# Kernel tuning notes

Measured on AMD Instinct MI355X. Metric: run time of the kernel, lower is better.

The kernel has to match this reference:

```python
import jax, jax.numpy as jnp
import numpy as np

N = 100_000      # nodes
E = 1_600_000    # edges (avg degree 16)
C_IN, C_H, C_OUT = 32, 64, 64
G = 64           # graphs in batch


def setup_inputs() -> dict:
    key = jax.random.key(0)
    ks = jax.random.split(key, 10)
    x = jax.random.normal(ks[0], (N, C_IN), jnp.float32)
    edge_index = jax.random.randint(ks[1], (2, E), 0, N, dtype=jnp.int64)
    edge_weight = jax.random.uniform(ks[2], (E,), jnp.float32)
    batch = jnp.sort(jax.random.randint(ks[3], (N,), 0, G, dtype=jnp.int64))
    def lin(k, fan_in, fan_out):
        return jax.random.normal(k, (fan_in, fan_out), jnp.float32) / np.float32(np.sqrt(fan_in))
    W1 = lin(ks[4], C_IN, C_H)
    W2 = lin(ks[5], C_H, C_H)
    W3 = lin(ks[6], C_H, C_OUT)
    b1 = jnp.zeros((C_H,), jnp.float32)
    b2 = jnp.zeros((C_H,), jnp.float32)
    b3 = jnp.zeros((C_OUT,), jnp.float32)
    return {"x": x, "edge_weight": edge_weight, "W1": W1, "b1": b1,
            "W2": W2, "b2": b2, "W3": W3, "b3": b3,
            "edge_index": edge_index, "batch": batch}


def _gcn_norm(edge_index, edge_weight, n):
    # PyG GCNConv default: add self-loops (weight 1), symmetric D^-1/2 A D^-1/2 norm.
    loop = jnp.arange(n, dtype=edge_index.dtype)
    src = jnp.concatenate([edge_index[0], loop])
    dst = jnp.concatenate([edge_index[1], loop])
    ew = jnp.concatenate([edge_weight, jnp.ones((n,), edge_weight.dtype)])
    deg = jax.ops.segment_sum(ew, dst, num_segments=n)
    dis = jnp.where(deg > 0, jax.lax.rsqrt(deg), jnp.float32(0))
    norm = dis[src] * ew * dis[dst]
    return src, dst, norm


def _gcn_layer(h, W, b, src, dst, norm, n):
    h = h @ W                                 # [N, out]
    msg = h[src] * norm[:, None]              # gather + scale  [E+N, out]
    agg = jax.ops.segment_sum(msg, dst, num_segments=n)
    return agg + b


def reference(x, edge_weight, W1, b1, W2, b2, W3, b3, edge_index, batch):
    n = x.shape[0]
    src, dst, norm = _gcn_norm(edge_index, edge_weight, n)  # shared across layers
    h = jax.nn.silu(_gcn_layer(x, W1, b1, src, dst, norm, n))
    # Dropout(0.1) is identity in eval mode
    h = jax.nn.silu(_gcn_layer(h, W2, b2, src, dst, norm, n))
    h = jax.nn.silu(_gcn_layer(h, W3, b3, src, dst, norm, n))
    # global_mean_pool over graphs
    sums = jax.ops.segment_sum(h, batch, num_segments=G)
    counts = jax.ops.segment_sum(jnp.ones((n,), h.dtype), batch, num_segments=G)
    return sums / jnp.maximum(counts, 1)[:, None]
```

## Files before the change

### kernel.cpp

```cpp
#include <hip/hip_runtime.h>
#include <hip/hip_fp16.h>
#include <math.h>


#define NB   256
#define PBLK 1024
#define FIXP_SCALE 1048576.0f
#define FIXP_MASK  ((1ULL << 40) - 1)

__device__ __forceinline__ int lower_bound_i(const int* __restrict__ a, int n, int v) {
    int lo = 0, hi = n;
    while (lo < hi) {
        int m = (lo + hi) >> 1;
        if (a[m] < v) lo = m + 1; else hi = m;
    }
    return lo;
}

__global__ __launch_bounds__(256) void k_bhist(const int* __restrict__ dst,
                                               int* __restrict__ hcnt, int e) {
    __shared__ int hist[NB];
    int tid = threadIdx.x, blk = blockIdx.x;
    hist[tid] = 0;
    __syncthreads();
    int chunk = (e + PBLK - 1) / PBLK;
    int lo = blk * chunk, hi = min(e, lo + chunk);
    for (int i = lo + tid; i < hi; i += 256)
        atomicAdd(&hist[dst[i] >> 9], 1);
    __syncthreads();
    hcnt[tid * PBLK + blk] = hist[tid];
}

__global__ __launch_bounds__(256) void k_bscan(int* __restrict__ hcnt,
                                               int* __restrict__ btot) {
    __shared__ int s[256];
    int b = blockIdx.x, tid = threadIdx.x;
    int* row = hcnt + b * PBLK;
    int a0 = row[4 * tid], a1 = row[4 * tid + 1], a2 = row[4 * tid + 2], a3 = row[4 * tid + 3];
    int tsum = a0 + a1 + a2 + a3;
    s[tid] = tsum;
    __syncthreads();
    for (int off = 1; off < 256; off <<= 1) {
        int t = (tid >= off) ? s[tid - off] : 0;
        __syncthreads();
        s[tid] += t;
        __syncthreads();
    }
    int ex = s[tid] - tsum;
    row[4 * tid] = ex;
    row[4 * tid + 1] = ex + a0;
    row[4 * tid + 2] = ex + a0 + a1;
    row[4 * tid + 3] = ex + a0 + a1 + a2;
    if (tid == 255) btot[b] = s[255];
}

__global__ __launch_bounds__(256) void k_bbase(const int* __restrict__ btot,
                                               int* __restrict__ bbase,
                                               int* __restrict__ rowptr, int n, int e) {
    __shared__ int s[256];
    int tid = threadIdx.x;
    int v = btot[tid];
    s[tid] = v;
    __syncthreads();
    for (int off = 1; off < 256; off <<= 1) {
        int t = (tid >= off) ? s[tid - off] : 0;
        __syncthreads();
        s[tid] += t;
        __syncthreads();
    }
    bbase[tid] = s[tid] - v;
    if (tid == 255) bbase[NB] = s[255];
    if (tid == 0) rowptr[n] = e;
}

__global__ __launch_bounds__(256) void k_bpart(const int* __restrict__ src,
                                               const int* __restrict__ dst,
                                               const float* __restrict__ ew,
                                               const int* __restrict__ hcnt,
                                               const int* __restrict__ bbase,
                                               int2* __restrict__ bedge, int e) {
    __shared__ int cur[NB];
    int tid = threadIdx.x, blk = blockIdx.x;
    cur[tid] = bbase[tid] + hcnt[tid * PBLK + blk];
    __syncthreads();
    int chunk = (e + PBLK - 1) / PBLK;
    int lo = blk * chunk, hi = min(e, lo + chunk);
    for (int i = lo + tid; i < hi; i += 256) {
        int d = dst[i];
        int pos = atomicAdd(&cur[d >> 9], 1);
        bedge[pos] = make_int2(src[i] | ((d & 511) << 17), __float_as_int(ew[i]));
    }
}

__global__ __launch_bounds__(256) void k_bucket(const int2* __restrict__ bedge,
                                                const int* __restrict__ bbase,
                                                float* __restrict__ dis,
                                                int* __restrict__ rowptr,
                                                int2* __restrict__ em, int n) {
    __shared__ unsigned long long pk[512];
    __shared__ int cnt[512];
    __shared__ int scn[512];
    __shared__ float sdis[512];
    __shared__ int cur[512];
    int b = blockIdx.x, tid = threadIdx.x;
    int e0 = bbase[b], e1 = bbase[b + 1];
    pk[tid] = 0ULL; pk[tid + 256] = 0ULL;
    __syncthreads();
    for (int i = e0 + tid; i < e1; i += 256) {
        int2 v = bedge[i];
        int dlo = (v.x >> 17) & 511;
        unsigned long long p =
            (1ULL << 40) | (unsigned long long)(__int_as_float(v.y) * FIXP_SCALE);
        atomicAdd(&pk[dlo], p);
    }
    __syncthreads();
#pragma unroll
    for (int k = 0; k < 2; ++k) {
        int i = tid + k * 256;
        unsigned long long v = pk[i];
        int c = (int)(v >> 40);
        cnt[i] = c; scn[i] = c;
        sdis[i] = rsqrtf(1.0f + (float)(v & FIXP_MASK) * (1.0f / FIXP_SCALE));
    }
    __syncthreads();
    for (int off = 1; off < 512; off <<= 1) {
        int i0 = tid, i1 = tid + 256;
        int v0 = (i0 >= off) ? scn[i0 - off] : 0;
        int v1 = (i1 >= off) ? scn[i1 - off] : 0;
        __syncthreads();
        scn[i0] += v0; scn[i1] += v1;
        __syncthreads();
    }
#pragma unroll
    for (int k = 0; k < 2; ++k) {
        int i = tid + k * 256;
        int rb = e0 + scn[i] - cnt[i];
        cur[i] = rb;
        int node = (b << 9) + i;
        if (node < n) { rowptr[node] = rb; dis[node] = sdis[i]; }
    }
    __syncthreads();
    for (int i = e0 + tid; i < e1; i += 256) {
        int2 v = bedge[i];
        int dlo = (v.x >> 17) & 511;
        int pos = atomicAdd(&cur[dlo], 1);
        float w = __int_as_float(v.y) * sdis[dlo];
        em[pos] = make_int2(v.x & 0x1FFFF, __float_as_int(w));
    }
}

__global__ void k_scale(const float* __restrict__ x, const float* __restrict__ dis,
                        __half* __restrict__ hs, int total) {
    int idx = blockIdx.x * blockDim.x + threadIdx.x;
    if (idx < total) hs[idx] = __float2half(x[idx] * dis[idx >> 5]);
}

__device__ __forceinline__ float2 cvt_pair(unsigned int u) {
    __half2 h2 = *(__half2*)&u;
    return __half22float2(h2);
}

__global__ __launch_bounds__(256, 2) void k_mm64(const __half* __restrict__ y,
                                                 const float* __restrict__ W,
                                                 __half* __restrict__ z, int n) {
    __shared__ float sw[64 * 64];
#pragma unroll
    for (int i = 0; i < 16; ++i)
        sw[threadIdx.x + 256 * i] = W[threadIdx.x + 256 * i];
    __syncthreads();
    int node = blockIdx.x * 256 + threadIdx.x;
    if (node >= n) return;
    uint4 yp[8];
    const uint4* yrow = (const uint4*)(y + (size_t)node * 64);
#pragma unroll
    for (int i = 0; i < 8; ++i) yp[i] = yrow[i];
    const unsigned int* ypk = (const unsigned int*)yp;
    float o[64];
#pragma unroll
    for (int j = 0; j < 64; ++j) o[j] = 0.0f;
#pragma unroll
    for (int k2 = 0; k2 < 32; ++k2) {
        float2 yk = cvt_pair(ypk[k2]);
        const float4* r0 = (const float4*)&sw[(2 * k2) * 64];
        const float4* r1 = (const float4*)&sw[(2 * k2 + 1) * 64];
#pragma unroll
        for (int j4 = 0; j4 < 16; ++j4) {
            float4 w0 = r0[j4];
            float4 w1 = r1[j4];
            o[4 * j4 + 0] = fmaf(yk.y, w1.x, fmaf(yk.x, w0.x, o[4 * j4 + 0]));
            o[4 * j4 + 1] = fmaf(yk.y, w1.y, fmaf(yk.x, w0.y, o[4 * j4 + 1]));
            o[4 * j4 + 2] = fmaf(yk.y, w1.z, fmaf(yk.x, w0.z, o[4 * j4 + 2]));
            o[4 * j4 + 3] = fmaf(yk.y, w1.w, fmaf(yk.x, w0.w, o[4 * j4 + 3]));
        }
    }
    __half2* zrow = (__half2*)(z + (size_t)node * 64);
#pragma unroll
    for (int j2 = 0; j2 < 32; ++j2)
        zrow[j2] = __float22half2_rn(make_float2(o[2 * j2], o[2 * j2 + 1]));
}

template <bool SCALE, typename OUT>
__global__ __launch_bounds__(256, 4) void k_agg64(const __half* __restrict__ z,
                                                  const int2* __restrict__ em,
                                                  const int* __restrict__ rowptr,
                                                  const float* __restrict__ dis,
                                                  const float* __restrict__ bias,
                                                  OUT* __restrict__ out, int n) {
    __shared__ __align__(8) int2 sme[4][64];
    int lane = threadIdx.x & 63, wv = threadIdx.x >> 6;
    int c = lane & 31, half = lane >> 5;
    const unsigned int* h32 = (const unsigned int*)z;
    float2 bv2 = ((const float2*)bias)[c];
    int wid = (blockIdx.x * blockDim.x + threadIdx.x) >> 6;
    int nw = (gridDim.x * blockDim.x) >> 6;
    for (int node = wid; node < n; node += nw) {
        int lo = rowptr[node], hi = rowptr[node + 1];
        int deg = hi - lo;
        float di = 0.0f;
        float2 acc = make_float2(0.0f, 0.0f);
        if (half == 0) {
            di = dis[node];
            float2 hv = cvt_pair(h32[(unsigned)(node * 32 + c)]);
            acc.x = di * hv.x; acc.y = di * hv.y;
        }
        for (int jb = 0; jb < deg; jb += 64) {
            int idx = lo + jb + lane;
            int2 me = (idx < hi) ? em[idx] : make_int2(0, 0);
            sme[wv][lane] = me;
            int rem = deg - jb;
#pragma unroll
            for (int g = 0; g < 4; ++g) {
                if (g * 16 < rem) {
                    int2 ev[8];
#pragma unroll
                    for (int t = 0; t < 8; ++t)
                        ev[t] = sme[wv][g * 16 + 2 * t + half];
                    unsigned int hv[8];
#pragma unroll
                    for (int t = 0; t < 8; ++t)
                        hv[t] = h32[(unsigned)(ev[t].x * 32 + c)];
#pragma unroll
                    for (int t = 0; t < 8; ++t) {
                        float ww = __int_as_float(ev[t].y);
                        float2 hf = cvt_pair(hv[t]);
                        acc.x = fmaf(ww, hf.x, acc.x);
                        acc.y = fmaf(ww, hf.y, acc.y);
                    }
                }
            }
        }
        acc.x += __shfl_down(acc.x, 32, 64);
        acc.y += __shfl_down(acc.y, 32, 64);
        if (half == 0) {
            float ox = acc.x + bv2.x, oy = acc.y + bv2.y;
            ox = ox / (1.0f + __expf(-ox));
            oy = oy / (1.0f + __expf(-oy));
            if (SCALE) { ox *= di; oy *= di; }
            if (sizeof(OUT) == 2) {
                ((__half2*)out)[(size_t)node * 32 + c] =
                    __float22half2_rn(make_float2(ox, oy));
            } else {
                ((float2*)out)[(size_t)node * 32 + c] = make_float2(ox, oy);
            }
        }
    }
}

__global__ __launch_bounds__(256, 3) void k_aggmm32(const __half* __restrict__ h,
                                                    const int2* __restrict__ em,
                                                    const int* __restrict__ rowptr,
                                                    const float* __restrict__ dis,
                                                    const float* __restrict__ W,
                                                    const float* __restrict__ bias,
                                                    __half* __restrict__ out, int n) {
    __shared__ __align__(16) float sacc[4][32];
    __shared__ __align__(8) int2 sme[4][64];
    int lane = threadIdx.x & 63, wv = threadIdx.x >> 6;
    int c = lane & 15, quarter = lane >> 4;
    const unsigned int* h32 = (const unsigned int*)h;
    float w[32];
#pragma unroll
    for (int k = 0; k < 32; ++k) w[k] = W[k * 64 + lane];
    float bv = bias[lane];
    int wid = (blockIdx.x * blockDim.x + threadIdx.x) >> 6;
    int nw = (gridDim.x * blockDim.x) >> 6;
    for (int node = wid; node < n; node += nw) {
#pragma unroll
        for (int k = 0; k < 32; ++k) asm volatile("" : "+v"(w[k]));
        int lo = rowptr[node], hi = rowptr[node + 1];
        int deg = hi - lo;
        float2 acc = make_float2(0.0f, 0.0f);
        if (quarter == 0) {
            float2 hv0 = cvt_pair(h32[(unsigned)(node * 16 + c)]);
            float di = dis[node];
            acc.x = di * hv0.x; acc.y = di * hv0.y;
        }
        for (int jb = 0; jb < deg; jb += 64) {
            int idx = lo + jb + lane;
            int2 me = (idx < hi) ? em[idx] : make_int2(0, 0);
            sme[wv][lane] = me;
            int rem = deg - jb;
#pragma unroll
            for (int g = 0; g < 4; ++g) {
                if (g * 16 < rem) {
                    int2 ev[4];
#pragma unroll
                    for (int t = 0; t < 4; ++t)
                        ev[t] = sme[wv][g * 16 + 4 * t + quarter];
                    unsigned int hv[4];
#pragma unroll
                    for (int t = 0; t < 4; ++t)
                        hv[t] = h32[(unsigned)(ev[t].x * 16 + c)];
#pragma unroll
                    for (int t = 0; t < 4; ++t) {
                        float ww = __int_as_float(ev[t].y);
                        float2 hf = cvt_pair(hv[t]);
                        acc.x = fmaf(ww, hf.x, acc.x);
                        acc.y = fmaf(ww, hf.y, acc.y);
                    }
                }
            }
        }
        acc.x += __shfl_down(acc.x, 32, 64);
        acc.y += __shfl_down(acc.y, 32, 64);
        acc.x += __shfl_down(acc.x, 16, 64);
        acc.y += __shfl_down(acc.y, 16, 64);
        if (quarter == 0) ((float2*)sacc[wv])[c] = acc;
        float o = bv;
        const float4* s4 = (const float4*)sacc[wv];
#pragma unroll
        for (int k4 = 0; k4 < 8; ++k4) {
            float4 a4 = s4[k4];
            o = fmaf(a4.x, w[4 * k4 + 0], o);
            o = fmaf(a4.y, w[4 * k4 + 1], o);
            o = fmaf(a4.z, w[4 * k4 + 2], o);
            o = fmaf(a4.w, w[4 * k4 + 3], o);
        }
        o = o / (1.0f + __expf(-o));
        o *= dis[node];
        out[(size_t)node * 64 + lane] = __float2half(o);
    }
}

__global__ void k_pool_partial(const float* __restrict__ h, const int* __restrict__ batch,
                               float* __restrict__ acc, int n) {
    int c = threadIdx.x & 63, r = threadIdx.x >> 6;
    int base = blockIdx.x * 128;
    int end = base + 128; if (end > n) end = n;
    float part = 0.0f;
    int cur = -1;
    for (int i = base + r; i < end; i += 4) {
        int g = batch[i];
        if (g != cur) {
            if (cur >= 0) atomicAdd(&acc[cur * 64 + c], part);
            part = 0.0f;
            cur = g;
        }
        part += h[(size_t)i * 64 + c];
    }
    if (cur >= 0) atomicAdd(&acc[cur * 64 + c], part);
}

__global__ void k_pool_final(const float* __restrict__ acc, const int* __restrict__ batch,
                             float* __restrict__ out, int n) {
    int idx = blockIdx.x * blockDim.x + threadIdx.x;
    int g = idx >> 6;
    int lo = lower_bound_i(batch, n, g);
    int hi = lower_bound_i(batch, n, g + 1);
    int cnt = hi - lo;
    out[idx] = acc[idx] / (float)(cnt > 0 ? cnt : 1);
}

extern "C" void kernel_launch(void* const* d_in, const int* in_sizes, int n_in,
                              void* d_out, int out_size, void* d_ws, size_t ws_size,
                              hipStream_t stream) {
    const float* x   = (const float*)d_in[0];
    const float* ew  = (const float*)d_in[1];
    const float* W1  = (const float*)d_in[2];
    const float* b1  = (const float*)d_in[3];
    const float* W2  = (const float*)d_in[4];
    const float* b2  = (const float*)d_in[5];
    const float* W3  = (const float*)d_in[6];
    const float* b3  = (const float*)d_in[7];
    const int*   eidx  = (const int*)d_in[8];
    const int*   batch = (const int*)d_in[9];
    float* out = (float*)d_out;

    const int E = in_sizes[1];
    const int N = in_sizes[9];
    const int G = 64;
    const int* src = eidx;
    const int* dst = eidx + E;

    char* p = (char*)d_ws;
    __half* A     = (__half*)p;                p += (size_t)N * 64 * sizeof(__half);
    __half* B     = (__half*)p;                p += (size_t)N * 64 * sizeof(__half);
    float* C      = (float*)p;                 p += (size_t)N * 64 * sizeof(float);
    float* dis    = (float*)p;                 p += (size_t)N * sizeof(float);
    int*   rowptr = (int*)p;                   p += (size_t)(N + 1) * sizeof(int);
    int*   bbase  = (int*)p;                   p += (size_t)(NB + 1) * sizeof(int);
    float* acc    = (float*)p;                 p += (size_t)G * 64 * sizeof(float);
    p = (char*)(((uintptr_t)p + 7) & ~(uintptr_t)7);
    int2*  em     = (int2*)p;

    int2* bedge = (int2*)A;
    int*  hcnt  = (int*)B;
    int*  btot  = (int*)B + NB * PBLK;

    const int BT = 256;
    const int FUSED_BLOCKS = 3125;
    const int MM_BLOCKS = (N + 255) / 256;

    k_bhist<<<PBLK, 256, 0, stream>>>(dst, hcnt, E);
    k_bscan<<<NB, 256, 0, stream>>>(hcnt, btot);
    k_bbase<<<1, 256, 0, stream>>>(btot, bbase, rowptr, N, E);
    k_bpart<<<PBLK, 256, 0, stream>>>(src, dst, ew, hcnt, bbase, bedge, E);
    k_bucket<<<NB, 256, 0, stream>>>(bedge, bbase, dis, rowptr, em, N);

    k_scale<<<(N * 32 + BT - 1) / BT, BT, 0, stream>>>(x, dis, (__half*)B, N * 32);
    k_aggmm32<<<FUSED_BLOCKS, BT, 0, stream>>>((__half*)B, em, rowptr, dis, W1, b1, A, N);

    k_mm64<<<MM_BLOCKS, BT, 0, stream>>>(A, W2, B, N);
    k_agg64<true, __half><<<FUSED_BLOCKS, BT, 0, stream>>>(B, em, rowptr, dis, b2, A, N);

    k_mm64<<<MM_BLOCKS, BT, 0, stream>>>(A, W3, B, N);
    k_agg64<false, float><<<FUSED_BLOCKS, BT, 0, stream>>>(B, em, rowptr, dis, b3, C, N);

    hipMemsetAsync(acc, 0, (size_t)G * 64 * sizeof(float), stream);
    k_pool_partial<<<(N + 127) / 128, BT, 0, stream>>>(C, batch, acc, N);
    k_pool_final<<<(G * 64) / BT, BT, 0, stream>>>(acc, batch, out, N);
}
```

Measured before the change: 355.8 us.

## Batch 8 consecutive nodes per wave with shared edge window; split layer-1 agg and matmul

Aggregation kernels now give each wave a contiguous run of 8 nodes. Row pointers are loaded once per wave, and a 128-entry edge window in shared memory is reused across node boundaries, so short adjacency lists no longer waste a whole 64-edge load per node. The fused layer-1 aggregate+matmul kernel is replaced by a separate 32-channel aggregation that writes fp16 to a scratch buffer, followed by a per-node matmul with bias, SiLU and degree scaling. The split adds an extra kernel launch and an intermediate round trip through memory, in exchange for removing the per-node register-resident weight dot product from the gather loop.

New measurement: 364.6 us. 1.02x slower.

```diff
diff --git a/kernel.cpp b/kernel.cpp
--- a/kernel.cpp
+++ b/kernel.cpp
@@ -160,26 +160,100 @@
     return __half22float2(h2);
 }
 
-__global__ __launch_bounds__(256, 2) void k_mm64(const __half* __restrict__ y,
-                                                 const float* __restrict__ W,
-                                                 __half* __restrict__ z, int n) {
-    __shared__ float sw[64 * 64];
-#pragma unroll
-    for (int i = 0; i < 16; ++i)
+__global__ __launch_bounds__(256, 4) void k_agg32(const __half* __restrict__ hs,
+                                                  const int2* __restrict__ em,
+                                                  const int* __restrict__ rowptr,
+                                                  const float* __restrict__ dis,
+                                                  __half* __restrict__ y0, int n) {
+    __shared__ __align__(8) int2 sme[4][128];
+    int lane = threadIdx.x & 63, wv = threadIdx.x >> 6;
+    int c = lane & 15, quarter = lane >> 4;
+    const unsigned int* h32 = (const unsigned int*)hs;
+    int wid = (blockIdx.x * blockDim.x + threadIdx.x) >> 6;
+    int n0 = wid * 8;
+    if (n0 >= n) return;
+    int cnt = min(8, n - n0);
+    int rp = 0;
+    if (lane <= cnt) rp = rowptr[n0 + lane];
+    int hiw = __shfl(rp, cnt, 64);
+    int wlo = 0, whi = 0;
+    for (int k = 0; k < cnt; ++k) {
+        int node = n0 + k;
+        int lo = __shfl(rp, k, 64), hi = __shfl(rp, k + 1, 64);
+        float2 acc = make_float2(0.0f, 0.0f);
+        if (quarter == 0) {
+            float di = dis[node];
+            float2 hv = cvt_pair(h32[(unsigned)(node * 16 + c)]);
+            acc.x = di * hv.x; acc.y = di * hv.y;
+        }
+        int idx = lo;
+        while (idx < hi) {
+            if (idx >= whi) {
+                int i0 = idx + lane;
+                if (i0 < hiw) sme[wv][lane] = em[i0];
+                if (idx + 64 < hiw) {
+                    int i1 = i0 + 64;
+                    if (i1 < hiw) sme[wv][lane + 64] = em[i1];
+                }
+                wlo = idx; whi = idx + 128;
+            }
+            int base = idx - wlo;
+            int take = min(hi, whi) - idx;
+            for (int g = 0; g < take; g += 16) {
+                int2 ev[4]; unsigned int hv[4]; int pr[4];
+#pragma unroll
+                for (int t = 0; t < 4; ++t) {
+                    int p = g + 4 * t + quarter;
+                    pr[t] = p < take;
+                    int pc = pr[t] ? p : 0;
+                    ev[t] = sme[wv][base + pc];
+                }
+#pragma unroll
+                for (int t = 0; t < 4; ++t)
+                    hv[t] = h32[(unsigned)(ev[t].x * 16 + c)];
+#pragma unroll
+                for (int t = 0; t < 4; ++t) {
+                    float ww = pr[t] ? __int_as_float(ev[t].y) : 0.0f;
+                    float2 hf = cvt_pair(hv[t]);
+                    acc.x = fmaf(ww, hf.x, acc.x);
+                    acc.y = fmaf(ww, hf.y, acc.y);
+                }
+            }
+            idx += take;
+        }
+        acc.x += __shfl_down(acc.x, 32, 64);
+        acc.y += __shfl_down(acc.y, 32, 64);
+        acc.x += __shfl_down(acc.x, 16, 64);
+        acc.y += __shfl_down(acc.y, 16, 64);
+        if (quarter == 0)
+            ((__half2*)y0)[(size_t)node * 16 + c] =
+                __float22half2_rn(make_float2(acc.x, acc.y));
+    }
+}
+
+__global__ __launch_bounds__(256, 2) void k_mm32act(const __half* __restrict__ y0,
+                                                    const float* __restrict__ W,
+                                                    const float* __restrict__ bias,
+                                                    const float* __restrict__ dis,
+                                                    __half* __restrict__ out, int n) {
+    __shared__ __align__(16) float sw[32 * 64 + 64];
+#pragma unroll
+    for (int i = 0; i < 8; ++i)
         sw[threadIdx.x + 256 * i] = W[threadIdx.x + 256 * i];
+    if (threadIdx.x < 64) sw[2048 + threadIdx.x] = bias[threadIdx.x];
     __syncthreads();
     int node = blockIdx.x * 256 + threadIdx.x;
     if (node >= n) return;
-    uint4 yp[8];
-    const uint4* yrow = (const uint4*)(y + (size_t)node * 64);
-#pragma unroll
-    for (int i = 0; i < 8; ++i) yp[i] = yrow[i];
+    uint4 yp[4];
+    const uint4* yrow = (const uint4*)(y0 + (size_t)node * 32);
+#pragma unroll
+    for (int i = 0; i < 4; ++i) yp[i] = yrow[i];
     const unsigned int* ypk = (const unsigned int*)yp;
     float o[64];
 #pragma unroll
-    for (int j = 0; j < 64; ++j) o[j] = 0.0f;
-#pragma unroll
-    for (int k2 = 0; k2 < 32; ++k2) {
+    for (int j = 0; j < 64; ++j) o[j] = sw[2048 + j];
+#pragma unroll
+    for (int k2 = 0; k2 < 16; ++k2) {
         float2 yk = cvt_pair(ypk[k2]);
         const float4* r0 = (const float4*)&sw[(2 * k2) * 64];
         const float4* r1 = (const float4*)&sw[(2 * k2 + 1) * 64];
@@ -193,6 +267,50 @@
             o[4 * j4 + 3] = fmaf(yk.y, w1.w, fmaf(yk.x, w0.w, o[4 * j4 + 3]));
         }
     }
+    float dsc = dis[node];
+    __half2* orow = (__half2*)(out + (size_t)node * 64);
+#pragma unroll
+    for (int j2 = 0; j2 < 32; ++j2) {
+        float ox = o[2 * j2], oy = o[2 * j2 + 1];
+        ox = ox / (1.0f + __expf(-ox)) * dsc;
+        oy = oy / (1.0f + __expf(-oy)) * dsc;
+        orow[j2] = __float22half2_rn(make_float2(ox, oy));
+    }
+}
+
+__global__ __launch_bounds__(256, 2) void k_mm64(const __half* __restrict__ y,
+                                                 const float* __restrict__ W,
+                                                 __half* __restrict__ z, int n) {
+    __shared__ __align__(16) float sw[64 * 64];
+#pragma unroll
+    for (int i = 0; i < 16; ++i)
+        sw[threadIdx.x + 256 * i] = W[threadIdx.x + 256 * i];
+    __syncthreads();
+    int node = blockIdx.x * 256 + threadIdx.x;
+    if (node >= n) return;
+    uint4 yp[8];
+    const uint4* yrow = (const uint4*)(y + (size_t)node * 64);
+#pragma unroll
+    for (int i = 0; i < 8; ++i) yp[i] = yrow[i];
+    const unsigned int* ypk = (const unsigned int*)yp;
+    float o[64];
+#pragma unroll
+    for (int j = 0; j < 64; ++j) o[j] = 0.0f;
+#pragma unroll
+    for (int k2 = 0; k2 < 32; ++k2) {
+        float2 yk = cvt_pair(ypk[k2]);
+        const float4* r0 = (const float4*)&sw[(2 * k2) * 64];
+        const float4* r1 = (const float4*)&sw[(2 * k2 + 1) * 64];
+#pragma unroll
+        for (int j4 = 0; j4 < 16; ++j4) {
+            float4 w0 = r0[j4];
+            float4 w1 = r1[j4];
+            o[4 * j4 + 0] = fmaf(yk.y, w1.x, fmaf(yk.x, w0.x, o[4 * j4 + 0]));
+            o[4 * j4 + 1] = fmaf(yk.y, w1.y, fmaf(yk.x, w0.y, o[4 * j4 + 1]));
+            o[4 * j4 + 2] = fmaf(yk.y, w1.z, fmaf(yk.x, w0.z, o[4 * j4 + 2]));
+            o[4 * j4 + 3] = fmaf(yk.y, w1.w, fmaf(yk.x, w0.w, o[4 * j4 + 3]));
+        }
+    }
     __half2* zrow = (__half2*)(z + (size_t)node * 64);
 #pragma unroll
     for (int j2 = 0; j2 < 32; ++j2)
@@ -206,16 +324,22 @@
                                                   const float* __restrict__ dis,
                                                   const float* __restrict__ bias,
                                                   OUT* __restrict__ out, int n) {
-    __shared__ __align__(8) int2 sme[4][64];
+    __shared__ __align__(8) int2 sme[4][128];
     int lane = threadIdx.x & 63, wv = threadIdx.x >> 6;
     int c = lane & 31, half = lane >> 5;
     const unsigned int* h32 = (const unsigned int*)z;
     float2 bv2 = ((const float2*)bias)[c];
     int wid = (blockIdx.x * blockDim.x + threadIdx.x) >> 6;
-    int nw = (gridDim.x * blockDim.x) >> 6;
-    for (int node = wid; node < n; node += nw) {
-        int lo = rowptr[node], hi = rowptr[node + 1];
-        int deg = hi - lo;
+    int n0 = wid * 8;
+    if (n0 >= n) return;
+    int cnt = min(8, n - n0);
+    int rp = 0;
+    if (lane <= cnt) rp = rowptr[n0 + lane];
+    int hiw = __shfl(rp, cnt, 64);
+    int wlo = 0, whi = 0;
+    for (int k = 0; k < cnt; ++k) {
+        int node = n0 + k;
+        int lo = __shfl(rp, k, 64), hi = __shfl(rp, k + 1, 64);
         float di = 0.0f;
         float2 acc = make_float2(0.0f, 0.0f);
         if (half == 0) {
@@ -223,31 +347,40 @@
             float2 hv = cvt_pair(h32[(unsigned)(node * 32 + c)]);
             acc.x = di * hv.x; acc.y = di * hv.y;
         }
-        for (int jb = 0; jb < deg; jb += 64) {
-            int idx = lo + jb + lane;
-            int2 me = (idx < hi) ? em[idx] : make_int2(0, 0);
-            sme[wv][lane] = me;
-            int rem = deg - jb;
-#pragma unroll
-            for (int g = 0; g < 4; ++g) {
-                if (g * 16 < rem) {
-                    int2 ev[8];
-#pragma unroll
-                    for (int t = 0; t < 8; ++t)
-                        ev[t] = sme[wv][g * 16 + 2 * t + half];
-                    unsigned int hv[8];
-#pragma unroll
-                    for (int t = 0; t < 8; ++t)
-                        hv[t] = h32[(unsigned)(ev[t].x * 32 + c)];
-#pragma unroll
-                    for (int t = 0; t < 8; ++t) {
-                        float ww = __int_as_float(ev[t].y);
-                        float2 hf = cvt_pair(hv[t]);
-                        acc.x = fmaf(ww, hf.x, acc.x);
-                        acc.y = fmaf(ww, hf.y, acc.y);
-                    }
-                }
+        int idx = lo;
+        while (idx < hi) {
+            if (idx >= whi) {
+                int i0 = idx + lane;
+                if (i0 < hiw) sme[wv][lane] = em[i0];
+                if (idx + 64 < hiw) {
+                    int i1 = i0 + 64;
+                    if (i1 < hiw) sme[wv][lane + 64] = em[i1];
+                }
+                wlo = idx; whi = idx + 128;
             }
+            int base = idx - wlo;
+            int take = min(hi, whi) - idx;
+            for (int g = 0; g < take; g += 16) {
+                int2 ev[8]; unsigned int hv[8]; int pr[8];
+#pragma unroll
+                for (int t = 0; t < 8; ++t) {
+                    int p = g + 2 * t + half;
+                    pr[t] = p < take;
+                    int pc = pr[t] ? p : 0;
+                    ev[t] = sme[wv][base + pc];
+                }
+#pragma unroll
+                for (int t = 0; t < 8; ++t)
+                    hv[t] = h32[(unsigned)(ev[t].x * 32 + c)];
+#pragma unroll
+                for (int t = 0; t < 8; ++t) {
+                    float ww = pr[t] ? __int_as_float(ev[t].y) : 0.0f;
+                    float2 hf = cvt_pair(hv[t]);
+                    acc.x = fmaf(ww, hf.x, acc.x);
+                    acc.y = fmaf(ww, hf.y, acc.y);
+                }
+            }
+            idx += take;
         }
         acc.x += __shfl_down(acc.x, 32, 64);
         acc.y += __shfl_down(acc.y, 32, 64);
@@ -263,82 +396,6 @@
                 ((float2*)out)[(size_t)node * 32 + c] = make_float2(ox, oy);
             }
         }
-    }
-}
-
-__global__ __launch_bounds__(256, 3) void k_aggmm32(const __half* __restrict__ h,
-                                                    const int2* __restrict__ em,
-                                                    const int* __restrict__ rowptr,
-                                                    const float* __restrict__ dis,
-                                                    const float* __restrict__ W,
-                                                    const float* __restrict__ bias,
-                                                    __half* __restrict__ out, int n) {
-    __shared__ __align__(16) float sacc[4][32];
-    __shared__ __align__(8) int2 sme[4][64];
-    int lane = threadIdx.x & 63, wv = threadIdx.x >> 6;
-    int c = lane & 15, quarter = lane >> 4;
-    const unsigned int* h32 = (const unsigned int*)h;
-    float w[32];
-#pragma unroll
-    for (int k = 0; k < 32; ++k) w[k] = W[k * 64 + lane];
-    float bv = bias[lane];
-    int wid = (blockIdx.x * blockDim.x + threadIdx.x) >> 6;
-    int nw = (gridDim.x * blockDim.x) >> 6;
-    for (int node = wid; node < n; node += nw) {
-#pragma unroll
-        for (int k = 0; k < 32; ++k) asm volatile("" : "+v"(w[k]));
-        int lo = rowptr[node], hi = rowptr[node + 1];
-        int deg = hi - lo;
-        float2 acc = make_float2(0.0f, 0.0f);
-        if (quarter == 0) {
-            float2 hv0 = cvt_pair(h32[(unsigned)(node * 16 + c)]);
-            float di = dis[node];
-            acc.x = di * hv0.x; acc.y = di * hv0.y;
-        }
-        for (int jb = 0; jb < deg; jb += 64) {
-            int idx = lo + jb + lane;
-            int2 me = (idx < hi) ? em[idx] : make_int2(0, 0);
-            sme[wv][lane] = me;
-            int rem = deg - jb;
-#pragma unroll
-            for (int g = 0; g < 4; ++g) {
-                if (g * 16 < rem) {
-                    int2 ev[4];
-#pragma unroll
-                    for (int t = 0; t < 4; ++t)
-                        ev[t] = sme[wv][g * 16 + 4 * t + quarter];
-                    unsigned int hv[4];
-#pragma unroll
-                    for (int t = 0; t < 4; ++t)
-                        hv[t] = h32[(unsigned)(ev[t].x * 16 + c)];
-#pragma unroll
-                    for (int t = 0; t < 4; ++t) {
-                        float ww = __int_as_float(ev[t].y);
-                        float2 hf = cvt_pair(hv[t]);
-                        acc.x = fmaf(ww, hf.x, acc.x);
-                        acc.y = fmaf(ww, hf.y, acc.y);
-                    }
-                }
-            }
-        }
-        acc.x += __shfl_down(acc.x, 32, 64);
-        acc.y += __shfl_down(acc.y, 32, 64);
-        acc.x += __shfl_down(acc.x, 16, 64);
-        acc.y += __shfl_down(acc.y, 16, 64);
-        if (quarter == 0) ((float2*)sacc[wv])[c] = acc;
-        float o = bv;
-        const float4* s4 = (const float4*)sacc[wv];
-#pragma unroll
-        for (int k4 = 0; k4 < 8; ++k4) {
-            float4 a4 = s4[k4];
-            o = fmaf(a4.x, w[4 * k4 + 0], o);
-            o = fmaf(a4.y, w[4 * k4 + 1], o);
-            o = fmaf(a4.z, w[4 * k4 + 2], o);
-            o = fmaf(a4.w, w[4 * k4 + 3], o);
-        }
-        o = o / (1.0f + __expf(-o));
-        o *= dis[node];
-        out[(size_t)node * 64 + lane] = __float2half(o);
     }
 }
 
@@ -408,7 +465,8 @@
     int*  btot  = (int*)B + NB * PBLK;
 
     const int BT = 256;
-    const int FUSED_BLOCKS = 3125;
+    const int WAVES = (N + 7) / 8;
+    const int AGG_BLOCKS = (WAVES + 3) / 4;
     const int MM_BLOCKS = (N + 255) / 256;
 
     k_bhist<<<PBLK, 256, 0, stream>>>(dst, hcnt, E);
@@ -418,13 +476,14 @@
     k_bucket<<<NB, 256, 0, stream>>>(bedge, bbase, dis, rowptr, em, N);
 
     k_scale<<<(N * 32 + BT - 1) / BT, BT, 0, stream>>>(x, dis, (__half*)B, N * 32);
-    k_aggmm32<<<FUSED_BLOCKS, BT, 0, stream>>>((__half*)B, em, rowptr, dis, W1, b1, A, N);
+    k_agg32<<<AGG_BLOCKS, BT, 0, stream>>>((__half*)B, em, rowptr, dis, (__half*)C, N);
+    k_mm32act<<<MM_BLOCKS, BT, 0, stream>>>((__half*)C, W1, b1, dis, A, N);
 
     k_mm64<<<MM_BLOCKS, BT, 0, stream>>>(A, W2, B, N);
-    k_agg64<true, __half><<<FUSED_BLOCKS, BT, 0, stream>>>(B, em, rowptr, dis, b2, A, N);
+    k_agg64<true, __half><<<AGG_BLOCKS, BT, 0, stream>>>(B, em, rowptr, dis, b2, A, N);
 
     k_mm64<<<MM_BLOCKS, BT, 0, stream>>>(A, W3, B, N);
-    k_agg64<false, float><<<FUSED_BLOCKS, BT, 0, stream>>>(B, em, rowptr, dis, b3, C, N);
+    k_agg64<false, float><<<AGG_BLOCKS, BT, 0, stream>>>(B, em, rowptr, dis, b3, C, N);
 
     hipMemsetAsync(acc, 0, (size_t)G * 64 * sizeof(float), stream);
     k_pool_partial<<<(N + 127) / 128, BT, 0, stream>>>(C, batch, acc, N);
```
